# Kernel optimization log

Hardware: AMD Instinct MI355X
Metric: run time of the kernel (lower is better)

The kernel has to match this reference:

```python
import jax, jax.numpy as jnp
import numpy as np

WIDTH = 384  # reconstruction grid is WIDTH x WIDTH


def _conv2d(x, w, b, pad):
    y = jax.lax.conv_general_dilated(
        x, w, window_strides=(1, 1), padding=[(pad, pad), (pad, pad)],
        dimension_numbers=('NCHW', 'OIHW', 'NCHW'))
    return y + b[None, :, None, None]


def _backproject(sino, angles, width):
    """Pixel-driven flat-detector fan-beam backprojection with linear interp.
    torch-radon FanBeam defaults: src_dist = det_dist = det_count,
    det_spacing = (src_dist + det_dist) / src_dist.
    sino: [B, C, A, D] -> image [B, C, width, width]."""
    B, C, A, D = sino.shape
    dsrc = float(D)
    ddet = float(D)
    spacing = (dsrc + ddet) / dsrc  # = 2.0
    c = jnp.arange(width, dtype=sino.dtype) - (width - 1) / 2.0
    X = c[None, None, :]   # [1,1,W] image x
    Y = c[None, :, None]   # [1,W,1] image y
    cb = jnp.cos(angles)[:, None, None]  # [A,1,1]
    sb = jnp.sin(angles)[:, None, None]
    px = cb * X + sb * Y    # pixel coords in rotated (source) frame, [A,W,W]
    py = -sb * X + cb * Y
    # fractional detector coordinate of the ray source->pixel
    s = px * ((dsrc + ddet) / spacing) / (dsrc + py) + (D - 1) / 2.0
    i0 = jnp.floor(s)
    frac = s - i0
    i0 = i0.astype(jnp.int32)
    i1 = i0 + 1
    WW = width * width
    w0 = jnp.where((i0 >= 0) & (i0 < D), 1.0 - frac, 0.0).reshape(A, WW)
    w1 = jnp.where((i1 >= 0) & (i1 < D), frac, 0.0).reshape(A, WW)
    i0c = jnp.clip(i0, 0, D - 1).reshape(A, WW)
    i1c = jnp.clip(i1, 0, D - 1).reshape(A, WW)

    def gather(idx):
        return jnp.take_along_axis(
            sino, jnp.broadcast_to(idx[None, None], (B, C, A, WW)), axis=3)

    out = (gather(i0c) * w0 + gather(i1c) * w1).sum(axis=2)  # sum over angles
    return out.reshape(B, C, width, width)


def setup_inputs() -> dict:
    key = jax.random.key(0)
    ks = jax.random.split(key, 5)
    A, D = 192, 576
    sino = jax.random.normal(ks[0], (1, 1, A, D), dtype=jnp.float32)
    angles = (jnp.arange(A, dtype=jnp.float32) * (2.0 * np.pi / A))
    w1 = jax.random.normal(ks[1], (16, 1, 5, 5), dtype=jnp.float32) * 0.05
    b1 = jnp.zeros((16,), dtype=jnp.float32)
    w2 = jax.random.normal(ks[2], (1, 16, 5, 5), dtype=jnp.float32) * 0.05
    b2 = jnp.zeros((1,), dtype=jnp.float32)
    w3 = jax.random.normal(ks[3], (1, 2, 3, 3), dtype=jnp.float32) * 0.05
    b3 = jnp.zeros((1,), dtype=jnp.float32)
    return {"sino": sino, "angles": angles, "w1": w1, "b1": b1,
            "w2": w2, "b2": b2, "w3": w3, "b3": b3}


def reference(sino, angles, w1, b1, w2, b2, w3, b3):
    img = _backproject(sino, angles, WIDTH)
    h = _conv2d(sino, w1, b1, pad=2)
    sino_pred = _conv2d(h, w2, b2, pad=2)
    img_sino = _backproject(sino_pred, angles, WIDTH)
    img_pred = _conv2d(jnp.concatenate([img, img_sino], axis=1), w3, b3, pad=1)
    return (sino_pred, img_sino, img_pred)
```

## Files before the change

### kernel.cpp

```cpp
#include <hip/hip_runtime.h>

#define A_N 192
#define D_N 576
#define W_N 384
#define NPIX (W_N * W_N)
#define NSIN (A_N * D_N)
#define RSTR 580

__global__ __launch_bounds__(256) void conv9_kernel(
    const float* __restrict__ sino, const float* __restrict__ angles,
    const float* __restrict__ w1, const float* __restrict__ b1,
    const float* __restrict__ w2, const float* __restrict__ b2,
    float* __restrict__ sino_pred, float2* __restrict__ inter,
    float4* __restrict__ tab)
{
    __shared__ float t[16][40];
    __shared__ float sw1[400], sw2[400], sb1[16];
    __shared__ float K[625], wsb1[25];
    __shared__ float Wcs[9][81];
    __shared__ float biasc[9];

    int tid = threadIdx.x;
    int byi = blockIdx.x / 18;
    int bxi = blockIdx.x % 18;
    int y0 = byi * 8, x0 = bxi * 32;

    if (blockIdx.x == 0) {
        if (tid < A_N) {
            float s, c;
            sincosf(angles[tid], &s, &c);
            tab[tid] = make_float4(c, s, fmaf(576.f, c, -287.5f * s),
                                         fmaf(576.f, s,  287.5f * c));
        }
        for (int i = tid; i < A_N * 4; i += 256) {
            int a = i >> 2, j = i & 3;
            inter[a * RSTR + (j < 2 ? j : 576 + j)] = make_float2(0.f, 0.f);
        }
    }

    for (int i = tid; i < 640; i += 256) {
        int r = i / 40, c = i - r * 40;
        int gy = y0 - 4 + r, gx = x0 - 4 + c;
        t[r][c] = (gy >= 0 && gy < A_N && gx >= 0 && gx < D_N)
                ? sino[gy * D_N + gx] : 0.f;
    }
    for (int i = tid; i < 400; i += 256) { sw1[i] = w1[i]; sw2[i] = w2[i]; }
    if (tid < 16) sb1[tid] = b1[tid];
    __syncthreads();

    for (int i = tid; i < 625; i += 256) {
        int q = i / 25, r = i - q * 25;
        float acc = 0.f;
        #pragma unroll
        for (int c = 0; c < 16; ++c)
            acc = fmaf(sw2[c * 25 + q], sw1[c * 25 + r], acc);
        K[i] = acc;
    }
    if (tid < 25) {
        float acc = 0.f;
        #pragma unroll
        for (int c = 0; c < 16; ++c) acc = fmaf(sw2[c * 25 + tid], sb1[c], acc);
        wsb1[tid] = acc;
    }
    __syncthreads();

    int ylo = (y0 == 0) ? 0 : 2, yhi = (y0 == A_N - 8) ? 4 : 2;
    int xlo = (x0 == 0) ? 0 : 2, xhi = (x0 == D_N - 32) ? 4 : 2;
    int nx = xhi - xlo + 1;
    int nc = (yhi - ylo + 1) * nx;

    for (int e = tid; e < nc * 81; e += 256) {
        int ci = e / 81, s = e - ci * 81;
        int yc = ylo + ci / nx, xc = xlo + ci % nx;
        int sy = s / 9 - 4, sx = s % 9 - 4;
        float acc = 0.f;
        for (int qy = -2; qy <= 2; ++qy) {
            if ((yc == 0 && qy < 0) || (yc == 1 && qy < -1) ||
                (yc == 3 && qy > 1) || (yc == 4 && qy > 0)) continue;
            int vy = sy - qy; if (vy < -2 || vy > 2) continue;
            for (int qx = -2; qx <= 2; ++qx) {
                if ((xc == 0 && qx < 0) || (xc == 1 && qx < -1) ||
                    (xc == 3 && qx > 1) || (xc == 4 && qx > 0)) continue;
                int vx = sx - qx; if (vx < -2 || vx > 2) continue;
                acc += K[((qy + 2) * 5 + qx + 2) * 25 + (vy + 2) * 5 + (vx + 2)];
            }
        }
        Wcs[ci][s] = acc;
    }
    if (tid < nc) {
        int yc = ylo + tid / nx, xc = xlo + tid % nx;
        float acc = b2[0];
        for (int qy = -2; qy <= 2; ++qy) {
            if ((yc == 0 && qy < 0) || (yc == 1 && qy < -1) ||
                (yc == 3 && qy > 1) || (yc == 4 && qy > 0)) continue;
            for (int qx = -2; qx <= 2; ++qx) {
                if ((xc == 0 && qx < 0) || (xc == 1 && qx < -1) ||
                    (xc == 3 && qx > 1) || (xc == 4 && qx > 0)) continue;
                acc += wsb1[(qy + 2) * 5 + qx + 2];
            }
        }
        biasc[tid] = acc;
    }
    __syncthreads();

    int lr = tid >> 5, lc = tid & 31;
    int gy = y0 + lr, gx = x0 + lc;
    int yc = (gy <= 1) ? gy : ((gy >= A_N - 2) ? (gy - (A_N - 5)) : 2);
    int xc = (gx <= 1) ? gx : ((gx >= D_N - 2) ? (gx - (D_N - 5)) : 2);
    int ci = (yc - ylo) * nx + (xc - xlo);
    float acc = biasc[ci];
    const float* Wp = Wcs[ci];
    #pragma unroll
    for (int sy = 0; sy < 9; ++sy)
        #pragma unroll
        for (int sx = 0; sx < 9; ++sx)
            acc = fmaf(t[lr + sy][lc + sx], Wp[sy * 9 + sx], acc);
    sino_pred[gy * D_N + gx] = acc;
    inter[gy * RSTR + 2 + gx] = make_float2(t[lr + 4][lc + 4], acc);
}

__global__ __launch_bounds__(256) void backproject2_kernel(
    const float2* __restrict__ inter, const float4* __restrict__ tab,
    float* __restrict__ part)
{
    int tid = threadIdx.x;
    int seg = blockIdx.z;
    int a0 = seg * 48;
    int tx = tid & 15, ty = tid >> 4;
    int gx = blockIdx.x * 16 + tx;
    int gy = blockIdx.y * 16 + ty;
    int idx = gy * W_N + gx;
    float X = (float)gx - 191.5f;
    float Y = (float)gy - 191.5f;
    float acc0 = 0.f, acc1 = 0.f;
    const float2* base = inter + (size_t)a0 * RSTR + 2;
    #pragma unroll 4
    for (int i = 0; i < 48; ++i) {
        float4 tb = tab[a0 + i];
        float den = fmaf(tb.x, Y, fmaf(-tb.y, X, 576.f));
        float num = fmaf(tb.z, X, fmaf(tb.w, Y, 165600.f));
        float s   = num * __builtin_amdgcn_rcpf(den);
        float fl  = floorf(s);
        float fr  = s - fl;
        int   ic  = min(max((int)fl, -2), 576);
        float4 v = *reinterpret_cast<const float4*>(base + (size_t)i * RSTR + ic);
        acc0 = fmaf(v.x, 1.f - fr, fmaf(v.z, fr, acc0));
        acc1 = fmaf(v.y, 1.f - fr, fmaf(v.w, fr, acc1));
    }
    part[seg * NPIX + idx]       = acc0;
    part[(4 + seg) * NPIX + idx] = acc1;
}

__global__ __launch_bounds__(256) void conv3_kernel(
    const float* __restrict__ part,
    const float* __restrict__ w3, const float* __restrict__ b3,
    float* __restrict__ img_sino, float* __restrict__ img_pred)
{
    __shared__ float t0[10][34], t1[10][34];
    __shared__ float sw[18];
    int tid = threadIdx.x;
    int byi = blockIdx.x / 12, bxi = blockIdx.x % 12;
    int y0 = byi * 8, x0 = bxi * 32;
    for (int i = tid; i < 340; i += 256) {
        int r = i / 34, c = i - r * 34;
        int gy = y0 - 1 + r, gx = x0 - 1 + c;
        float s0 = 0.f, s1 = 0.f;
        if (gy >= 0 && gy < W_N && gx >= 0 && gx < W_N) {
            int g = gy * W_N + gx;
            #pragma unroll
            for (int p = 0; p < 4; ++p) s0 += part[p * NPIX + g];
            #pragma unroll
            for (int p = 4; p < 8; ++p) s1 += part[p * NPIX + g];
        }
        t0[r][c] = s0; t1[r][c] = s1;
    }
    if (tid < 18) sw[tid] = w3[tid];
    __syncthreads();
    int lr = tid >> 5, lc = tid & 31;
    int gy = y0 + lr, gx = x0 + lc;
    int g = gy * W_N + gx;
    img_sino[g] = t1[lr + 1][lc + 1];
    float acc = b3[0];
    #pragma unroll
    for (int dy = 0; dy < 3; ++dy)
        #pragma unroll
        for (int dx = 0; dx < 3; ++dx) {
            acc = fmaf(t0[lr + dy][lc + dx], sw[dy * 3 + dx], acc);
            acc = fmaf(t1[lr + dy][lc + dx], sw[9 + dy * 3 + dx], acc);
        }
    img_pred[g] = acc;
}

extern "C" void kernel_launch(void* const* d_in, const int* in_sizes, int n_in,
                              void* d_out, int out_size, void* d_ws, size_t ws_size,
                              hipStream_t stream) {
    const float* sino   = (const float*)d_in[0];
    const float* angles = (const float*)d_in[1];
    const float* w1     = (const float*)d_in[2];
    const float* b1     = (const float*)d_in[3];
    const float* w2     = (const float*)d_in[4];
    const float* b2     = (const float*)d_in[5];
    const float* w3     = (const float*)d_in[6];
    const float* b3     = (const float*)d_in[7];

    float* out       = (float*)d_out;
    float* sino_pred = out;
    float* img_sino  = out + NSIN;
    float* img_pred  = img_sino + NPIX;

    float2* inter = (float2*)d_ws;
    float4* tab   = (float4*)((char*)d_ws + (size_t)A_N * RSTR * sizeof(float2));
    float*  part  = (float*)((char*)tab + A_N * sizeof(float4));

    conv9_kernel<<<dim3(432), dim3(256), 0, stream>>>(
        sino, angles, w1, b1, w2, b2, sino_pred, inter, tab);
    backproject2_kernel<<<dim3(24, 24, 4), dim3(256), 0, stream>>>(
        inter, tab, part);
    conv3_kernel<<<dim3(576), dim3(256), 0, stream>>>(
        part, w3, b3, img_sino, img_pred);
}
```

Measured before the change: 37.16 us.

## Overlap raw-sinogram backprojection with conv stage in one fused launch

Moves the backprojection of the raw sinogram out of the second kernel and into extra blocks of the first kernel. Those blocks compute their own angle table and read the sinogram directly with bounds-masked weights. The second kernel now backprojects only the predicted sinogram from a scalar padded buffer, so it does half the gathers. The intent is to fill idle CUs during the small conv launch and cut the dependent backprojection work. The cost is a larger first grid and duplicated trig work per block.

```diff
diff --git a/kernel.cpp b/kernel.cpp
--- a/kernel.cpp
+++ b/kernel.cpp
@@ -7,133 +7,169 @@
 #define NSIN (A_N * D_N)
 #define RSTR 580
 
-__global__ __launch_bounds__(256) void conv9_kernel(
+__global__ __launch_bounds__(256) void k1_kernel(
     const float* __restrict__ sino, const float* __restrict__ angles,
     const float* __restrict__ w1, const float* __restrict__ b1,
     const float* __restrict__ w2, const float* __restrict__ b2,
-    float* __restrict__ sino_pred, float2* __restrict__ inter,
-    float4* __restrict__ tab)
+    float* __restrict__ sino_pred, float* __restrict__ inter,
+    float4* __restrict__ tab, float* __restrict__ part)
 {
-    __shared__ float t[16][40];
-    __shared__ float sw1[400], sw2[400], sb1[16];
-    __shared__ float K[625], wsb1[25];
-    __shared__ float Wcs[9][81];
-    __shared__ float biasc[9];
-
     int tid = threadIdx.x;
-    int byi = blockIdx.x / 18;
-    int bxi = blockIdx.x % 18;
-    int y0 = byi * 8, x0 = bxi * 32;
-
-    if (blockIdx.x == 0) {
-        if (tid < A_N) {
+    if (blockIdx.x < 432) {
+        __shared__ float t[16][40];
+        __shared__ float sw1[400], sw2[400], sb1[16];
+        __shared__ float K[625], wsb1[25];
+        __shared__ float Wcs[9][81];
+        __shared__ float biasc[9];
+
+        int byi = blockIdx.x / 18;
+        int bxi = blockIdx.x % 18;
+        int y0 = byi * 8, x0 = bxi * 32;
+
+        if (blockIdx.x == 0) {
+            if (tid < A_N) {
+                float s, c;
+                sincosf(angles[tid], &s, &c);
+                tab[tid] = make_float4(c, s, fmaf(576.f, c, -287.5f * s),
+                                             fmaf(576.f, s,  287.5f * c));
+            }
+            for (int i = tid; i < A_N * 4; i += 256) {
+                int a = i >> 2, j = i & 3;
+                inter[a * RSTR + (j < 2 ? j : 576 + j)] = 0.f;
+            }
+        }
+
+        for (int i = tid; i < 640; i += 256) {
+            int r = i / 40, c = i - r * 40;
+            int gy = y0 - 4 + r, gx = x0 - 4 + c;
+            t[r][c] = (gy >= 0 && gy < A_N && gx >= 0 && gx < D_N)
+                    ? sino[gy * D_N + gx] : 0.f;
+        }
+        for (int i = tid; i < 400; i += 256) { sw1[i] = w1[i]; sw2[i] = w2[i]; }
+        if (tid < 16) sb1[tid] = b1[tid];
+        __syncthreads();
+
+        for (int i = tid; i < 625; i += 256) {
+            int q = i / 25, r = i - q * 25;
+            float acc = 0.f;
+            #pragma unroll
+            for (int c = 0; c < 16; ++c)
+                acc = fmaf(sw2[c * 25 + q], sw1[c * 25 + r], acc);
+            K[i] = acc;
+        }
+        if (tid < 25) {
+            float acc = 0.f;
+            #pragma unroll
+            for (int c = 0; c < 16; ++c)
+                acc = fmaf(sw2[c * 25 + tid], sb1[c], acc);
+            wsb1[tid] = acc;
+        }
+        __syncthreads();
+
+        int ylo = (y0 == 0) ? 0 : 2, yhi = (y0 == A_N - 8) ? 4 : 2;
+        int xlo = (x0 == 0) ? 0 : 2, xhi = (x0 == D_N - 32) ? 4 : 2;
+        int nx = xhi - xlo + 1;
+        int nc = (yhi - ylo + 1) * nx;
+
+        for (int e = tid; e < nc * 81; e += 256) {
+            int ci = e / 81, s = e - ci * 81;
+            int yc = ylo + ci / nx, xc = xlo + ci % nx;
+            int sy = s / 9 - 4, sx = s % 9 - 4;
+            float acc = 0.f;
+            for (int qy = -2; qy <= 2; ++qy) {
+                if ((yc == 0 && qy < 0) || (yc == 1 && qy < -1) ||
+                    (yc == 3 && qy > 1) || (yc == 4 && qy > 0)) continue;
+                int vy = sy - qy; if (vy < -2 || vy > 2) continue;
+                for (int qx = -2; qx <= 2; ++qx) {
+                    if ((xc == 0 && qx < 0) || (xc == 1 && qx < -1) ||
+                        (xc == 3 && qx > 1) || (xc == 4 && qx > 0)) continue;
+                    int vx = sx - qx; if (vx < -2 || vx > 2) continue;
+                    acc += K[((qy + 2) * 5 + qx + 2) * 25 + (vy + 2) * 5 + (vx + 2)];
+                }
+            }
+            Wcs[ci][s] = acc;
+        }
+        if (tid < nc) {
+            int yc = ylo + tid / nx, xc = xlo + tid % nx;
+            float acc = b2[0];
+            for (int qy = -2; qy <= 2; ++qy) {
+                if ((yc == 0 && qy < 0) || (yc == 1 && qy < -1) ||
+                    (yc == 3 && qy > 1) || (yc == 4 && qy > 0)) continue;
+                for (int qx = -2; qx <= 2; ++qx) {
+                    if ((xc == 0 && qx < 0) || (xc == 1 && qx < -1) ||
+                        (xc == 3 && qx > 1) || (xc == 4 && qx > 0)) continue;
+                    acc += wsb1[(qy + 2) * 5 + qx + 2];
+                }
+            }
+            biasc[tid] = acc;
+        }
+        __syncthreads();
+
+        int lr = tid >> 5, lc = tid & 31;
+        int gy = y0 + lr, gx = x0 + lc;
+        int yc = (gy <= 1) ? gy : ((gy >= A_N - 2) ? (gy - (A_N - 5)) : 2);
+        int xc = (gx <= 1) ? gx : ((gx >= D_N - 2) ? (gx - (D_N - 5)) : 2);
+        int ci = (yc - ylo) * nx + (xc - xlo);
+        float acc = biasc[ci];
+        const float* Wp = Wcs[ci];
+        #pragma unroll
+        for (int sy = 0; sy < 9; ++sy)
+            #pragma unroll
+            for (int sx = 0; sx < 9; ++sx)
+                acc = fmaf(t[lr + sy][lc + sx], Wp[sy * 9 + sx], acc);
+        sino_pred[gy * D_N + gx] = acc;
+        inter[gy * RSTR + 2 + gx] = acc;
+    } else {
+        __shared__ float4 tl[48];
+        int b = blockIdx.x - 432;
+        int seg = b / 576;
+        int r   = b % 576;
+        int a0  = seg * 48;
+        if (tid < 48) {
             float s, c;
-            sincosf(angles[tid], &s, &c);
-            tab[tid] = make_float4(c, s, fmaf(576.f, c, -287.5f * s),
-                                         fmaf(576.f, s,  287.5f * c));
-        }
-        for (int i = tid; i < A_N * 4; i += 256) {
-            int a = i >> 2, j = i & 3;
-            inter[a * RSTR + (j < 2 ? j : 576 + j)] = make_float2(0.f, 0.f);
-        }
+            sincosf(angles[a0 + tid], &s, &c);
+            tl[tid] = make_float4(c, s, fmaf(576.f, c, -287.5f * s),
+                                        fmaf(576.f, s,  287.5f * c));
+        }
+        __syncthreads();
+        int gx = (r % 24) * 16 + (tid & 15);
+        int gy = (r / 24) * 16 + (tid >> 4);
+        float X = (float)gx - 191.5f;
+        float Y = (float)gy - 191.5f;
+        float acc = 0.f;
+        #pragma unroll 4
+        for (int i = 0; i < 48; ++i) {
+            float4 tb = tl[i];
+            float den = fmaf(tb.x, Y, fmaf(-tb.y, X, 576.f));
+            float num = fmaf(tb.z, X, fmaf(tb.w, Y, 165600.f));
+            float s   = num * __builtin_amdgcn_rcpf(den);
+            float fl  = floorf(s);
+            float fr  = s - fl;
+            int i0 = (int)fl, i1 = i0 + 1;
+            float w0 = ((unsigned)i0 < 576u) ? (1.f - fr) : 0.f;
+            float w1 = ((unsigned)i1 < 576u) ? fr : 0.f;
+            int i0c = min(max(i0, 0), 575);
+            int i1c = min(max(i1, 0), 575);
+            const float* row = sino + (a0 + i) * D_N;
+            acc = fmaf(row[i0c], w0, fmaf(row[i1c], w1, acc));
+        }
+        part[seg * NPIX + gy * W_N + gx] = acc;
     }
-
-    for (int i = tid; i < 640; i += 256) {
-        int r = i / 40, c = i - r * 40;
-        int gy = y0 - 4 + r, gx = x0 - 4 + c;
-        t[r][c] = (gy >= 0 && gy < A_N && gx >= 0 && gx < D_N)
-                ? sino[gy * D_N + gx] : 0.f;
-    }
-    for (int i = tid; i < 400; i += 256) { sw1[i] = w1[i]; sw2[i] = w2[i]; }
-    if (tid < 16) sb1[tid] = b1[tid];
-    __syncthreads();
-
-    for (int i = tid; i < 625; i += 256) {
-        int q = i / 25, r = i - q * 25;
-        float acc = 0.f;
-        #pragma unroll
-        for (int c = 0; c < 16; ++c)
-            acc = fmaf(sw2[c * 25 + q], sw1[c * 25 + r], acc);
-        K[i] = acc;
-    }
-    if (tid < 25) {
-        float acc = 0.f;
-        #pragma unroll
-        for (int c = 0; c < 16; ++c) acc = fmaf(sw2[c * 25 + tid], sb1[c], acc);
-        wsb1[tid] = acc;
-    }
-    __syncthreads();
-
-    int ylo = (y0 == 0) ? 0 : 2, yhi = (y0 == A_N - 8) ? 4 : 2;
-    int xlo = (x0 == 0) ? 0 : 2, xhi = (x0 == D_N - 32) ? 4 : 2;
-    int nx = xhi - xlo + 1;
-    int nc = (yhi - ylo + 1) * nx;
-
-    for (int e = tid; e < nc * 81; e += 256) {
-        int ci = e / 81, s = e - ci * 81;
-        int yc = ylo + ci / nx, xc = xlo + ci % nx;
-        int sy = s / 9 - 4, sx = s % 9 - 4;
-        float acc = 0.f;
-        for (int qy = -2; qy <= 2; ++qy) {
-            if ((yc == 0 && qy < 0) || (yc == 1 && qy < -1) ||
-                (yc == 3 && qy > 1) || (yc == 4 && qy > 0)) continue;
-            int vy = sy - qy; if (vy < -2 || vy > 2) continue;
-            for (int qx = -2; qx <= 2; ++qx) {
-                if ((xc == 0 && qx < 0) || (xc == 1 && qx < -1) ||
-                    (xc == 3 && qx > 1) || (xc == 4 && qx > 0)) continue;
-                int vx = sx - qx; if (vx < -2 || vx > 2) continue;
-                acc += K[((qy + 2) * 5 + qx + 2) * 25 + (vy + 2) * 5 + (vx + 2)];
-            }
-        }
-        Wcs[ci][s] = acc;
-    }
-    if (tid < nc) {
-        int yc = ylo + tid / nx, xc = xlo + tid % nx;
-        float acc = b2[0];
-        for (int qy = -2; qy <= 2; ++qy) {
-            if ((yc == 0 && qy < 0) || (yc == 1 && qy < -1) ||
-                (yc == 3 && qy > 1) || (yc == 4 && qy > 0)) continue;
-            for (int qx = -2; qx <= 2; ++qx) {
-                if ((xc == 0 && qx < 0) || (xc == 1 && qx < -1) ||
-                    (xc == 3 && qx > 1) || (xc == 4 && qx > 0)) continue;
-                acc += wsb1[(qy + 2) * 5 + qx + 2];
-            }
-        }
-        biasc[tid] = acc;
-    }
-    __syncthreads();
-
-    int lr = tid >> 5, lc = tid & 31;
-    int gy = y0 + lr, gx = x0 + lc;
-    int yc = (gy <= 1) ? gy : ((gy >= A_N - 2) ? (gy - (A_N - 5)) : 2);
-    int xc = (gx <= 1) ? gx : ((gx >= D_N - 2) ? (gx - (D_N - 5)) : 2);
-    int ci = (yc - ylo) * nx + (xc - xlo);
-    float acc = biasc[ci];
-    const float* Wp = Wcs[ci];
-    #pragma unroll
-    for (int sy = 0; sy < 9; ++sy)
-        #pragma unroll
-        for (int sx = 0; sx < 9; ++sx)
-            acc = fmaf(t[lr + sy][lc + sx], Wp[sy * 9 + sx], acc);
-    sino_pred[gy * D_N + gx] = acc;
-    inter[gy * RSTR + 2 + gx] = make_float2(t[lr + 4][lc + 4], acc);
-}
-
-__global__ __launch_bounds__(256) void backproject2_kernel(
-    const float2* __restrict__ inter, const float4* __restrict__ tab,
+}
+
+__global__ __launch_bounds__(256) void bpb_kernel(
+    const float* __restrict__ inter, const float4* __restrict__ tab,
     float* __restrict__ part)
 {
     int tid = threadIdx.x;
     int seg = blockIdx.z;
     int a0 = seg * 48;
-    int tx = tid & 15, ty = tid >> 4;
-    int gx = blockIdx.x * 16 + tx;
-    int gy = blockIdx.y * 16 + ty;
-    int idx = gy * W_N + gx;
+    int gx = blockIdx.x * 16 + (tid & 15);
+    int gy = blockIdx.y * 16 + (tid >> 4);
     float X = (float)gx - 191.5f;
     float Y = (float)gy - 191.5f;
-    float acc0 = 0.f, acc1 = 0.f;
-    const float2* base = inter + (size_t)a0 * RSTR + 2;
+    float acc = 0.f;
+    const float* base = inter + (size_t)a0 * RSTR + 2;
     #pragma unroll 4
     for (int i = 0; i < 48; ++i) {
         float4 tb = tab[a0 + i];
@@ -143,12 +179,10 @@
         float fl  = floorf(s);
         float fr  = s - fl;
         int   ic  = min(max((int)fl, -2), 576);
-        float4 v = *reinterpret_cast<const float4*>(base + (size_t)i * RSTR + ic);
-        acc0 = fmaf(v.x, 1.f - fr, fmaf(v.z, fr, acc0));
-        acc1 = fmaf(v.y, 1.f - fr, fmaf(v.w, fr, acc1));
+        float2 v = *reinterpret_cast<const float2*>(base + (size_t)i * RSTR + ic);
+        acc = fmaf(v.x, 1.f - fr, fmaf(v.y, fr, acc));
     }
-    part[seg * NPIX + idx]       = acc0;
-    part[(4 + seg) * NPIX + idx] = acc1;
+    part[(4 + seg) * NPIX + gy * W_N + gx] = acc;
 }
 
 __global__ __launch_bounds__(256) void conv3_kernel(
@@ -208,13 +242,13 @@
     float* img_sino  = out + NSIN;
     float* img_pred  = img_sino + NPIX;
 
-    float2* inter = (float2*)d_ws;
-    float4* tab   = (float4*)((char*)d_ws + (size_t)A_N * RSTR * sizeof(float2));
+    float*  inter = (float*)d_ws;
+    float4* tab   = (float4*)((char*)d_ws + (size_t)A_N * RSTR * 4);
     float*  part  = (float*)((char*)tab + A_N * sizeof(float4));
 
-    conv9_kernel<<<dim3(432), dim3(256), 0, stream>>>(
-        sino, angles, w1, b1, w2, b2, sino_pred, inter, tab);
-    backproject2_kernel<<<dim3(24, 24, 4), dim3(256), 0, stream>>>(
+    k1_kernel<<<dim3(2736), dim3(256), 0, stream>>>(
+        sino, angles, w1, b1, w2, b2, sino_pred, inter, tab, part);
+    bpb_kernel<<<dim3(24, 24, 4), dim3(256), 0, stream>>>(
         inter, tab, part);
     conv3_kernel<<<dim3(576), dim3(256), 0, stream>>>(
         part, w3, b3, img_sino, img_pred);
```

New measurement: 44.41 us. 1.2x slower.
